# Kernel tuning notes

Hardware: AMD Instinct MI355X
Metric: run time of the kernel (lower is better)

The kernel has to match this reference:

```python
import jax, jax.numpy as jnp
from jax import lax
import numpy as np

DIM, DT_RANK, D_INNER, D_STATE = 256, 16, 256, 16

def _ssm_params(key, d, dt_rank, d_inner, n):
    k1, k2, k3 = jax.random.split(key, 3)
    Wdbc = jax.random.normal(k1, (d, dt_rank + 2 * n), jnp.float32) * 0.02
    Wdt = jax.random.normal(k2, (dt_rank, d_inner), jnp.float32) * 0.02
    bdt = jax.random.normal(k3, (d_inner,), jnp.float32) * 0.02
    Alog = jnp.log(jnp.tile(jnp.arange(1, n + 1, dtype=jnp.float32), (d_inner, 1)))
    D = jnp.ones((d_inner,), jnp.float32)
    return Wdbc, Wdt, bdt, Alog, D

def setup_inputs() -> dict:
    key = jax.random.key(0)
    ks = jax.random.split(key, 10)
    x = jax.random.normal(ks[0], (4, 4096, DIM), jnp.float32)
    ln_g = jnp.ones((DIM,), jnp.float32)
    ln_b = jnp.zeros((DIM,), jnp.float32)
    Wp = jax.random.normal(ks[1], (DIM, DIM), jnp.float32) * 0.02
    bp = jnp.zeros((DIM,), jnp.float32)
    Wcf = jax.random.normal(ks[2], (DIM, DIM), jnp.float32) * 0.02  # conv1d k=1 == pointwise matmul
    bcf = jnp.zeros((DIM,), jnp.float32)
    Wcb = jax.random.normal(ks[3], (DIM, DIM), jnp.float32) * 0.02
    bcb = jnp.zeros((DIM,), jnp.float32)
    Wdbc_f, Wdt_f, bdt_f, Alog_f, D_f = _ssm_params(ks[4], DIM, DT_RANK, D_INNER, D_STATE)
    Wdbc_b, Wdt_b, bdt_b, Alog_b, D_b = _ssm_params(ks[5], DIM, DT_RANK, D_INNER, D_STATE)
    return dict(x=x, ln_g=ln_g, ln_b=ln_b, Wp=Wp, bp=bp, Wcf=Wcf, bcf=bcf, Wcb=Wcb, bcb=bcb,
                Wdbc_f=Wdbc_f, Wdt_f=Wdt_f, bdt_f=bdt_f, Alog_f=Alog_f, D_f=D_f,
                Wdbc_b=Wdbc_b, Wdt_b=Wdt_b, bdt_b=bdt_b, Alog_b=Alog_b, D_b=D_b)

def _layernorm(x, g, b, eps=1e-5):
    mu = jnp.mean(x, -1, keepdims=True)
    var = jnp.var(x, -1, keepdims=True)
    return (x - mu) * lax.rsqrt(var + eps) * g + b

def _selective_scan(x, delta, A, B, C, D):
    # x, delta: [b,s,d]; A: [d,n]; B, C: [b,s,n]; D: [d]
    deltaA = jnp.exp(delta[..., None] * A)              # [b,s,d,n]
    BX = delta[..., None] * B[:, :, None, :] * x[..., None]  # [b,s,d,n]
    dA = jnp.moveaxis(deltaA, 1, 0)
    bx = jnp.moveaxis(BX, 1, 0)
    def step(h, inp):
        dA_t, bx_t = inp
        h = dA_t * h + bx_t
        return h, h
    h0 = jnp.zeros_like(dA[0])
    _, hs = lax.scan(step, h0, (dA, bx))                # [s,b,d,n]
    hs = jnp.moveaxis(hs, 0, 1)                          # [b,s,d,n]
    y = jnp.einsum('bsdn,bsn->bsd', hs, C) + D * x
    return y

def _ssm(x, Wdbc, Wdt, bdt, Alog, D):
    A = -jnp.exp(Alog)
    dbc = x @ Wdbc
    dt_r, B, C = jnp.split(dbc, [DT_RANK, DT_RANK + D_STATE], axis=-1)
    delta = jax.nn.softplus(dt_r @ Wdt + bdt)
    return _selective_scan(x, delta, A, B, C, D)

def _process(x, Wc, bc, Wdbc, Wdt, bdt, Alog, D):
    x = jax.nn.softplus(x @ Wc.T + bc)  # Conv1d k=1: out[e] = sum_d W[e,d] x[d] + b[e]
    return _ssm(x, Wdbc, Wdt, bdt, Alog, D)

def reference(x, ln_g, ln_b, Wp, bp, Wcf, bcf, Wcb, bcb,
              Wdbc_f, Wdt_f, bdt_f, Alog_f, D_f,
              Wdbc_b, Wdt_b, bdt_b, Alog_b, D_b):
    skip = x
    xn = _layernorm(x, ln_g, ln_b)
    z1 = xn @ Wp + bp  # proj used for both z1 and x (same layer twice)
    xp = z1
    x1 = jax.nn.silu(_process(xp, Wcf, bcf, Wdbc_f, Wdt_f, bdt_f, Alog_f, D_f))
    x2r = _process(jnp.flip(xp, 1), Wcb, bcb, Wdbc_b, Wdt_b, bdt_b, Alog_b, D_b)
    x2 = jax.nn.silu(jnp.flip(x2r, 1))
    z = jax.nn.silu(z1)
    return x1 * z + x2 * z + skip
```

## Files before the change

### kernel.cpp

```cpp
#include <hip/hip_runtime.h>
#include <math.h>

#define SB 4
#define SS 4096
#define SD 256
#define SN 16
#define ROWS 16
#define NRB 1024
#define NCH 128
#define CHL 32

#define BM 128
#define BN 64
#define BK 64
#define LDT 72

#define MBM 64
#define MLDZ 264
#define MLDT 72
#define MLDE 68

typedef __attribute__((ext_vector_type(8))) short bf16x8;
typedef __attribute__((ext_vector_type(4))) float f32x4;

__device__ __forceinline__ unsigned short f2bf(float f){
    unsigned int u = __float_as_uint(f);
    u += 0x7FFFu + ((u >> 16) & 1u);
    return (unsigned short)(u >> 16);
}
__device__ __forceinline__ float bf2f(unsigned short u){
    return __uint_as_float(((unsigned int)u) << 16);
}
__device__ __forceinline__ float softplus_f(float x){
    return fmaxf(x, 0.f) + __logf(1.f + __expf(-fabsf(x)));
}
__device__ __forceinline__ float silu_f(float x){
    return x * __builtin_amdgcn_rcpf(1.f + __expf(-x));
}

__global__ __launch_bounds__(256)
void k_prep(const float* __restrict__ Wp,
            const float* __restrict__ Wcf, const float* __restrict__ Wcb,
            const float* __restrict__ Wdbc0, const float* __restrict__ Wdt0,
            const float* __restrict__ Wdbc1, const float* __restrict__ Wdt1,
            unsigned short* __restrict__ WpT, unsigned short* __restrict__ Wc,
            unsigned short* __restrict__ G3W)
{
    int idx = blockIdx.x*256 + threadIdx.x;
    if (idx < 65536){
        int n = idx >> 8, k = idx & 255;
        WpT[idx] = f2bf(Wp[k*256 + n]);
    } else if (idx < 65536 + 131072){
        int j = idx - 65536;
        Wc[j] = f2bf(j < 65536 ? Wcf[j] : Wcb[j - 65536]);
    } else {
        int j = idx - 196608;
        int dir = j / 81920; int r = j - dir*81920;
        int n = r >> 8, d = r & 255;
        const float* Wdbc = dir ? Wdbc1 : Wdbc0;
        const float* Wdt  = dir ? Wdt1  : Wdt0;
        float v;
        if (n < 256){
            v = 0.f;
            #pragma unroll
            for (int q = 0; q < 16; ++q)
                v = fmaf(Wdbc[d*48 + q], Wdt[q*256 + n], v);
        } else if (n < 272) v = Wdbc[d*48 + 16 + (n-256)];
        else if (n < 288)   v = Wdbc[d*48 + 32 + (n-272)];
        else                v = 0.f;
        G3W[(size_t)dir*81920 + r] = f2bf(v);
    }
}

__global__ __launch_bounds__(256)
void k_ln(const float* __restrict__ x, const float* __restrict__ g,
          const float* __restrict__ bln, unsigned short* __restrict__ xnbf){
    int row0 = blockIdx.x * ROWS;
    int tid = threadIdx.x; int w = tid >> 6; int lane = tid & 63;
    #pragma unroll
    for (int rep = 0; rep < 4; ++rep){
        int j = rep*4 + w;
        const float* xr = x + (size_t)(row0 + j)*SD;
        float4 v = *(const float4*)(xr + lane*4);
        float s = v.x + v.y + v.z + v.w;
        #pragma unroll
        for (int off = 32; off; off >>= 1) s += __shfl_xor(s, off, 64);
        float mu = s * (1.f/256.f);
        float d0 = v.x-mu, d1 = v.y-mu, d2 = v.z-mu, d3 = v.w-mu;
        float q = d0*d0 + d1*d1 + d2*d2 + d3*d3;
        #pragma unroll
        for (int off = 32; off; off >>= 1) q += __shfl_xor(q, off, 64);
        float rstd = rsqrtf(q*(1.f/256.f) + 1e-5f);
        float4 gg = *(const float4*)(g + lane*4);
        float4 bb = *(const float4*)(bln + lane*4);
        ushort4 o;
        o.x = f2bf(d0*rstd*gg.x + bb.x);
        o.y = f2bf(d1*rstd*gg.y + bb.y);
        o.z = f2bf(d2*rstd*gg.z + bb.z);
        o.w = f2bf(d3*rstd*gg.w + bb.w);
        *(ushort4*)(xnbf + (size_t)(row0+j)*SD + lane*4) = o;
    }
}

__global__ __launch_bounds__(256, 5)
void k_gemm0(const unsigned short* __restrict__ A,
             const unsigned short* __restrict__ Bt,
             const float* __restrict__ bias0,
             unsigned short* __restrict__ obf)
{
    __shared__ unsigned short sMem[(BM + BN) * LDT];
    unsigned short (*sA)[LDT] = (unsigned short (*)[LDT])sMem;
    unsigned short (*sB)[LDT] = (unsigned short (*)[LDT])(sMem + BM*LDT);
    int ntile = blockIdx.x, mtile = blockIdx.y;
    int row0 = mtile * BM;
    int col0 = ntile * BN;

    int tid = threadIdx.x;
    uint4 ra[4], rb[2];
    auto gload = [&](int kt){
        int k0 = kt * BK;
        #pragma unroll
        for (int i = 0; i < 4; ++i){
            int idx = tid + i*256; int r = idx >> 3, kp = idx & 7;
            ra[i] = *(const uint4*)(A + (size_t)(row0 + r)*256 + k0 + kp*8);
        }
        #pragma unroll
        for (int i = 0; i < 2; ++i){
            int idx = tid + i*256; int r = idx >> 3, kp = idx & 7;
            rb[i] = *(const uint4*)(Bt + (size_t)(col0 + r)*256 + k0 + kp*8);
        }
    };
    auto swrite = [&](){
        #pragma unroll
        for (int i = 0; i < 4; ++i){
            int idx = tid + i*256; int r = idx >> 3, kp = idx & 7;
            *(uint4*)&sA[r][kp*8] = ra[i];
        }
        #pragma unroll
        for (int i = 0; i < 2; ++i){
            int idx = tid + i*256; int r = idx >> 3, kp = idx & 7;
            *(uint4*)&sB[r][kp*8] = rb[i];
        }
    };

    gload(0); swrite(); __syncthreads();

    int lane = tid & 63, w = tid >> 6;
    int wr = w >> 1, wc = w & 1;
    int lr = lane & 15, hi = lane >> 4;

    f32x4 acc[4][2];
    #pragma unroll
    for (int mf = 0; mf < 4; ++mf)
        #pragma unroll
        for (int nf = 0; nf < 2; ++nf)
            acc[mf][nf] = f32x4{0.f, 0.f, 0.f, 0.f};

    for (int kt = 0; kt < 4; ++kt){
        if (kt < 3) gload(kt + 1);
        #pragma unroll
        for (int kk = 0; kk < BK; kk += 32){
            bf16x8 af[4], bfr[2];
            #pragma unroll
            for (int mf = 0; mf < 4; ++mf)
                af[mf] = *(const bf16x8*)&sA[wr*64 + mf*16 + lr][kk + hi*8];
            #pragma unroll
            for (int nf = 0; nf < 2; ++nf)
                bfr[nf] = *(const bf16x8*)&sB[wc*32 + nf*16 + lr][kk + hi*8];
            #pragma unroll
            for (int mf = 0; mf < 4; ++mf)
                #pragma unroll
                for (int nf = 0; nf < 2; ++nf)
                    acc[mf][nf] = __builtin_amdgcn_mfma_f32_16x16x32_bf16(
                        af[mf], bfr[nf], acc[mf][nf], 0, 0, 0);
        }
        if (kt < 3){
            __syncthreads();
            swrite();
            __syncthreads();
        }
    }

    __syncthreads();
    unsigned short (*sOut)[LDT] = (unsigned short (*)[LDT])sMem;
    #pragma unroll
    for (int mf = 0; mf < 4; ++mf){
        #pragma unroll
        for (int nf = 0; nf < 2; ++nf){
            int col = col0 + wc*32 + nf*16 + lr;
            float bias = bias0[col];
            #pragma unroll
            for (int r = 0; r < 4; ++r)
                sOut[wr*64 + mf*16 + hi*4 + r][wc*32 + nf*16 + lr] =
                    f2bf(acc[mf][nf][r] + bias);
        }
    }
    __syncthreads();
    #pragma unroll
    for (int p = 0; p < 4; ++p){
        int chunk = tid + p*256;
        int r = chunk >> 3, cg = chunk & 7;
        uint4 v = *(const uint4*)&sOut[r][cg*8];
        *(uint4*)(obf + (size_t)(row0 + r)*256 + col0 + cg*8) = v;
    }
}

__global__ __launch_bounds__(256, 2)
void k_mid(const unsigned short* __restrict__ z1bf,
           const unsigned short* __restrict__ Wc,
           const unsigned short* __restrict__ G3W,
           const float* __restrict__ bc0, const float* __restrict__ bc1,
           const float* __restrict__ bdt0, const float* __restrict__ bdt1,
           unsigned short* __restrict__ xcbf,
           unsigned short* __restrict__ dg0, unsigned short* __restrict__ dg1,
           float* __restrict__ Bg0, float* __restrict__ Bg1,
           float* __restrict__ Cg0, float* __restrict__ Cg1)
{
    __shared__ unsigned short sZ[MBM*MLDZ];
    __shared__ unsigned short sX[MBM*MLDT];
    int mtile = blockIdx.x, dir = blockIdx.y;
    int row0 = mtile*MBM;
    int tid = threadIdx.x;
    int lane = tid & 63, w = tid >> 6;
    int wr = w >> 1, wc = w & 1;
    int lr = lane & 15, hi = lane >> 4;

    {
        const uint4* src = (const uint4*)(z1bf + (size_t)row0*256);
        #pragma unroll
        for (int p = 0; p < 8; ++p){
            int idx = tid + p*256;
            int r = idx >> 5, cq = idx & 31;
            *(uint4*)&sZ[r*MLDZ + cq*8] = src[idx];
        }
    }
    __syncthreads();

    const float* bcp  = dir ? bc1  : bc0;
    const float* bdtp = dir ? bdt1 : bdt0;
    unsigned short* dgp = dir ? dg1 : dg0;
    const unsigned short* Wcp = Wc + (size_t)dir*65536;
    const unsigned short* Gp  = G3W + (size_t)dir*81920;

    f32x4 acc2[5][2][2];
    #pragma unroll
    for (int t5 = 0; t5 < 5; ++t5)
        #pragma unroll
        for (int mf = 0; mf < 2; ++mf)
            #pragma unroll
            for (int nf = 0; nf < 2; ++nf)
                acc2[t5][mf][nf] = f32x4{0.f,0.f,0.f,0.f};

    #pragma unroll 1
    for (int nt1 = 0; nt1 < 4; ++nt1){
        f32x4 acc1[2][2];
        #pragma unroll
        for (int mf = 0; mf < 2; ++mf)
            #pragma unroll
            for (int nf = 0; nf < 2; ++nf)
                acc1[mf][nf] = f32x4{0.f,0.f,0.f,0.f};
        #pragma unroll
        for (int kt = 0; kt < 4; ++kt){
            #pragma unroll
            for (int kk = 0; kk < 64; kk += 32){
                bf16x8 wf0 = *(const bf16x8*)(Wcp + (size_t)(nt1*64 + wc*32 +      lr)*256 + kt*64 + kk + hi*8);
                bf16x8 wf1 = *(const bf16x8*)(Wcp + (size_t)(nt1*64 + wc*32 + 16 + lr)*256 + kt*64 + kk + hi*8);
                bf16x8 zf0 = *(const bf16x8*)&sZ[(wr*32 +      lr)*MLDZ + kt*64 + kk + hi*8];
                bf16x8 zf1 = *(const bf16x8*)&sZ[(wr*32 + 16 + lr)*MLDZ + kt*64 + kk + hi*8];
                acc1[0][0] = __builtin_amdgcn_mfma_f32_16x16x32_bf16(wf0, zf0, acc1[0][0], 0,0,0);
                acc1[0][1] = __builtin_amdgcn_mfma_f32_16x16x32_bf16(wf1, zf0, acc1[0][1], 0,0,0);
                acc1[1][0] = __builtin_amdgcn_mfma_f32_16x16x32_bf16(wf0, zf1, acc1[1][0], 0,0,0);
                acc1[1][1] = __builtin_amdgcn_mfma_f32_16x16x32_bf16(wf1, zf1, acc1[1][1], 0,0,0);
            }
        }
        __syncthreads();
        #pragma unroll
        for (int mf = 0; mf < 2; ++mf){
            #pragma unroll
            for (int nf = 0; nf < 2; ++nf){
                float4 bb = *(const float4*)(bcp + nt1*64 + wc*32 + nf*16 + hi*4);
                ushort4 o;
                o.x = f2bf(softplus_f(acc1[mf][nf][0] + bb.x));
                o.y = f2bf(softplus_f(acc1[mf][nf][1] + bb.y));
                o.z = f2bf(softplus_f(acc1[mf][nf][2] + bb.z));
                o.w = f2bf(softplus_f(acc1[mf][nf][3] + bb.w));
                *(ushort4*)&sX[(wr*32 + mf*16 + lr)*MLDT + wc*32 + nf*16 + hi*4] = o;
            }
        }
        __syncthreads();
        #pragma unroll
        for (int p = 0; p < 2; ++p){
            int idx = tid + p*256; int r = idx>>3, c8 = idx&7;
            *(uint4*)(xcbf + (size_t)(row0 + r)*512 + dir*256 + nt1*64 + c8*8) =
                *(const uint4*)&sX[r*MLDT + c8*8];
        }
        bf16x8 af[2][2];
        #pragma unroll
        for (int mf = 0; mf < 2; ++mf)
            #pragma unroll
            for (int k2 = 0; k2 < 2; ++k2)
                af[mf][k2] = *(const bf16x8*)&sX[(wr*32 + mf*16 + lr)*MLDT + k2*32 + hi*8];
        #pragma unroll
        for (int nt2 = 0; nt2 < 5; ++nt2){
            #pragma unroll
            for (int k2 = 0; k2 < 2; ++k2){
                bf16x8 gf0 = *(const bf16x8*)(Gp + (size_t)(nt2*64 + wc*32 +      lr)*256 + nt1*64 + k2*32 + hi*8);
                bf16x8 gf1 = *(const bf16x8*)(Gp + (size_t)(nt2*64 + wc*32 + 16 + lr)*256 + nt1*64 + k2*32 + hi*8);
                acc2[nt2][0][0] = __builtin_amdgcn_mfma_f32_16x16x32_bf16(af[0][k2], gf0, acc2[nt2][0][0], 0,0,0);
                acc2[nt2][0][1] = __builtin_amdgcn_mfma_f32_16x16x32_bf16(af[0][k2], gf1, acc2[nt2][0][1], 0,0,0);
                acc2[nt2][1][0] = __builtin_amdgcn_mfma_f32_16x16x32_bf16(af[1][k2], gf0, acc2[nt2][1][0], 0,0,0);
                acc2[nt2][1][1] = __builtin_amdgcn_mfma_f32_16x16x32_bf16(af[1][k2], gf1, acc2[nt2][1][1], 0,0,0);
            }
        }
    }

    float* sE = (float*)sZ;
    #pragma unroll
    for (int nt2 = 0; nt2 < 5; ++nt2){
        __syncthreads();
        #pragma unroll
        for (int mf = 0; mf < 2; ++mf)
            #pragma unroll
            for (int nf = 0; nf < 2; ++nf)
                #pragma unroll
                for (int r = 0; r < 4; ++r)
                    sE[(wr*32 + mf*16 + hi*4 + r)*MLDE + wc*32 + nf*16 + lr] =
                        acc2[nt2][mf][nf][r];
        __syncthreads();
        if (nt2 < 4){
            #pragma unroll
            for (int p = 0; p < 2; ++p){
                int idx = tid + p*256; int r = idx>>3, c8 = idx&7;
                float4 v0 = *(const float4*)&sE[r*MLDE + c8*8];
                float4 v1 = *(const float4*)&sE[r*MLDE + c8*8 + 4];
                int col = nt2*64 + c8*8;
                float4 b0 = *(const float4*)(bdtp + col);
                float4 b1 = *(const float4*)(bdtp + col + 4);
                ushort4 o0, o1;
                o0.x = f2bf(softplus_f(v0.x + b0.x));
                o0.y = f2bf(softplus_f(v0.y + b0.y));
                o0.z = f2bf(softplus_f(v0.z + b0.z));
                o0.w = f2bf(softplus_f(v0.w + b0.w));
                o1.x = f2bf(softplus_f(v1.x + b1.x));
                o1.y = f2bf(softplus_f(v1.y + b1.y));
                o1.z = f2bf(softplus_f(v1.z + b1.z));
                o1.w = f2bf(softplus_f(v1.w + b1.w));
                ushort4 pk[2] = {o0, o1};
                *(uint4*)(dgp + (size_t)(row0 + r)*SD + col) = *(const uint4*)pk;
            }
        } else {
            float* Bp = dir ? Bg1 : Bg0;
            float* Cp = dir ? Cg1 : Cg0;
            int r = tid >> 2, q = tid & 3;
            float4 bv = *(const float4*)&sE[r*MLDE + q*4];
            float4 cv = *(const float4*)&sE[r*MLDE + 16 + q*4];
            *(float4*)(Bp + (size_t)(row0 + r)*SN + q*4) = bv;
            *(float4*)(Cp + (size_t)(row0 + r)*SN + q*4) = cv;
        }
    }
}

__global__ __launch_bounds__(256)
void k_scan_p1(const unsigned short* __restrict__ xcbf,
               const unsigned short* __restrict__ dg0, const float* __restrict__ B0, const float* __restrict__ Al0,
               const unsigned short* __restrict__ dg1, const float* __restrict__ B1, const float* __restrict__ Al1,
               float* __restrict__ hend, float* __restrict__ sdl)
{
    __shared__ float sB[CHL*SN];
    int blk = blockIdx.x;
    int c = blk & (NCH-1); int dir = (blk>>7) & 1; int b = blk>>8;
    const unsigned short* dg = dir ? dg1 : dg0;
    const float* Bg   = dir ? B1  : B0;
    const float* Alog = dir ? Al1 : Al0;
    const unsigned short* xc = xcbf + dir*256;
    int d = threadIdx.x;
    #pragma unroll
    for (int k = 0; k < 2; ++k){
        int li = threadIdx.x + k*256;
        int i = li >> 4, n = li & 15;
        int tau = c*CHL + i;
        int t = dir ? (SS-1-tau) : tau;
        sB[li] = Bg[((size_t)b*SS + t)*SN + n];
    }
    float A[SN];
    #pragma unroll
    for (int k = 0; k < 4; ++k){
        float4 al = *(const float4*)(Alog + d*SN + k*4);
        A[k*4+0] = -__expf(al.x); A[k*4+1] = -__expf(al.y);
        A[k*4+2] = -__expf(al.z); A[k*4+3] = -__expf(al.w);
    }
    __syncthreads();
    int t0 = dir ? (SS-1 - c*CHL) : (c*CHL);
    const unsigned short* pd = dg + ((size_t)b*SS + t0)*SD + d;
    const unsigned short* px = xc + ((size_t)b*SS + t0)*512 + d;
    int strided = dir ? -SD : SD;
    int stridex = dir ? -512 : 512;
    float h[SN];
    #pragma unroll
    for (int n = 0; n < SN; ++n) h[n] = 0.f;
    float sumdl = 0.f;
    float dl = bf2f(*pd), xv = bf2f(*px);
    for (int i = 0; i < CHL; ++i){
        float dlN = 0.f, xvN = 0.f;
        if (i+1 < CHL){ pd += strided; px += stridex; dlN = bf2f(*pd); xvN = bf2f(*px); }
        sumdl += dl;
        float dlx = dl * xv;
        const float4* b4 = (const float4*)&sB[i*SN];
        #pragma unroll
        for (int k = 0; k < 4; ++k){
            float4 bb = b4[k];
            h[k*4+0] = fmaf(__expf(dl*A[k*4+0]), h[k*4+0], bb.x*dlx);
            h[k*4+1] = fmaf(__expf(dl*A[k*4+1]), h[k*4+1], bb.y*dlx);
            h[k*4+2] = fmaf(__expf(dl*A[k*4+2]), h[k*4+2], bb.z*dlx);
            h[k*4+3] = fmaf(__expf(dl*A[k*4+3]), h[k*4+3], bb.w*dlx);
        }
        dl = dlN; xv = xvN;
    }
    size_t base = (((size_t)(b*2+dir)*NCH + c)*SD + d)*SN;
    #pragma unroll
    for (int k = 0; k < 4; ++k)
        *(float4*)(hend + base + k*4) = make_float4(h[k*4+0],h[k*4+1],h[k*4+2],h[k*4+3]);
    sdl[((size_t)(b*2+dir)*NCH + c)*SD + d] = sumdl;
}

__global__ __launch_bounds__(256)
void k_chain(const float* __restrict__ Al0, const float* __restrict__ Al1,
             float* hend, const float* __restrict__ sdl)
{
    int gidx = blockIdx.x*256 + threadIdx.x;
    int n = gidx & 15; int d = (gidx >> 4) & 255; int dirb = gidx >> 12;
    const float* Alog = (dirb & 1) ? Al1 : Al0;
    float A = -__expf(Alog[d*SN + n]);
    float H = 0.f;
    const size_t cs = (size_t)SD*SN;
    size_t idx  = (size_t)dirb*NCH*cs + (size_t)d*SN + n;
    size_t sidx = (size_t)dirb*NCH*SD + d;
    float he[4], sd[4];
    #pragma unroll
    for (int k = 0; k < 4; ++k){
        he[k] = hend[idx + (size_t)k*cs];
        sd[k] = sdl[sidx + (size_t)k*SD];
    }
    for (int cg = 0; cg < NCH; cg += 4){
        float heN[4] = {0.f,0.f,0.f,0.f};
        float sdN[4] = {0.f,0.f,0.f,0.f};
        if (cg + 4 < NCH){
            #pragma unroll
            for (int k = 0; k < 4; ++k){
                heN[k] = hend[idx + (size_t)(k+4)*cs];
                sdN[k] = sdl[sidx + (size_t)(k+4)*SD];
            }
        }
        #pragma unroll
        for (int k = 0; k < 4; ++k){
            hend[idx + (size_t)k*cs] = H;
            H = fmaf(__expf(A*sd[k]), H, he[k]);
        }
        #pragma unroll
        for (int k = 0; k < 4; ++k){ he[k] = heN[k]; sd[k] = sdN[k]; }
        idx += 4*cs; sidx += 4*SD;
    }
}

__global__ __launch_bounds__(256)
void k_scan_p2f(const unsigned short* __restrict__ xcbf,
                const unsigned short* __restrict__ dg0, const float* __restrict__ B0,
                const float* __restrict__ C0, const float* __restrict__ Al0,
                const float* __restrict__ Dv0,
                const unsigned short* __restrict__ dg1, const float* __restrict__ B1,
                const float* __restrict__ C1, const float* __restrict__ Al1,
                const float* __restrict__ Dv1,
                const float* __restrict__ hin,
                const unsigned short* __restrict__ z1bf,
                const float* __restrict__ x,
                float* __restrict__ out)
{
    __shared__ float yL[CHL*SD];
    __shared__ float sB0[CHL*SN], sC0[CHL*SN], sB1[CHL*SN], sC1[CHL*SN];
    int blk = blockIdx.x;
    int c = blk & (NCH-1); int b = blk >> 7;
    int d = threadIdx.x;
    #pragma unroll
    for (int k = 0; k < 2; ++k){
        int li = threadIdx.x + k*256;
        int i = li >> 4, n = li & 15;
        int tF = c*CHL + i;
        int tR = c*CHL + (CHL-1) - i;
        sB0[li] = B0[((size_t)b*SS + tF)*SN + n];
        sC0[li] = C0[((size_t)b*SS + tF)*SN + n];
        sB1[li] = B1[((size_t)b*SS + tR)*SN + n];
        sC1[li] = C1[((size_t)b*SS + tR)*SN + n];
    }
    __syncthreads();

    {
        float A[SN];
        #pragma unroll
        for (int k = 0; k < 4; ++k){
            float4 al = *(const float4*)(Al0 + d*SN + k*4);
            A[k*4+0] = -__expf(al.x); A[k*4+1] = -__expf(al.y);
            A[k*4+2] = -__expf(al.z); A[k*4+3] = -__expf(al.w);
        }
        float h[SN];
        size_t base = (((size_t)(b*2+0)*NCH + c)*SD + d)*SN;
        #pragma unroll
        for (int k = 0; k < 4; ++k){
            float4 hv = *(const float4*)(hin + base + k*4);
            h[k*4+0]=hv.x; h[k*4+1]=hv.y; h[k*4+2]=hv.z; h[k*4+3]=hv.w;
        }
        float Dd = Dv0[d];
        for (int i = 0; i < CHL; ++i){
            size_t rowb = (size_t)b*SS + c*CHL + i;
            float dl = bf2f(dg0[rowb*SD + d]);
            float xv = bf2f(xcbf[rowb*512 + d]);
            float dlx = dl * xv;
            float yv = Dd * xv;
            const float4* b4 = (const float4*)&sB0[i*SN];
            const float4* c4 = (const float4*)&sC0[i*SN];
            #pragma unroll
            for (int k = 0; k < 4; ++k){
                float4 bb = b4[k];
                float4 cc = c4[k];
                h[k*4+0] = fmaf(__expf(dl*A[k*4+0]), h[k*4+0], bb.x*dlx);
                yv = fmaf(h[k*4+0], cc.x, yv);
                h[k*4+1] = fmaf(__expf(dl*A[k*4+1]), h[k*4+1], bb.y*dlx);
                yv = fmaf(h[k*4+1], cc.y, yv);
                h[k*4+2] = fmaf(__expf(dl*A[k*4+2]), h[k*4+2], bb.z*dlx);
                yv = fmaf(h[k*4+2], cc.z, yv);
                h[k*4+3] = fmaf(__expf(dl*A[k*4+3]), h[k*4+3], bb.w*dlx);
                yv = fmaf(h[k*4+3], cc.w, yv);
            }
            yL[i*SD + d] = yv;
        }
    }
    {
        float A[SN];
        #pragma unroll
        for (int k = 0; k < 4; ++k){
            float4 al = *(const float4*)(Al1 + d*SN + k*4);
            A[k*4+0] = -__expf(al.x); A[k*4+1] = -__expf(al.y);
            A[k*4+2] = -__expf(al.z); A[k*4+3] = -__expf(al.w);
        }
        float h[SN];
        size_t base = (((size_t)(b*2+1)*NCH + (NCH-1-c))*SD + d)*SN;
        #pragma unroll
        for (int k = 0; k < 4; ++k){
            float4 hv = *(const float4*)(hin + base + k*4);
            h[k*4+0]=hv.x; h[k*4+1]=hv.y; h[k*4+2]=hv.z; h[k*4+3]=hv.w;
        }
        float Dd = Dv1[d];
        for (int ip = 0; ip < CHL; ++ip){
            int iloc = (CHL-1) - ip;
            size_t rowb = (size_t)b*SS + c*CHL + iloc;
            float dl = bf2f(dg1[rowb*SD + d]);
            float xv = bf2f(xcbf[rowb*512 + 256 + d]);
            float dlx = dl * xv;
            float yv = Dd * xv;
            const float4* b4 = (const float4*)&sB1[ip*SN];
            const float4* c4 = (const float4*)&sC1[ip*SN];
            #pragma unroll
            for (int k = 0; k < 4; ++k){
                float4 bb = b4[k];
                float4 cc = c4[k];
                h[k*4+0] = fmaf(__expf(dl*A[k*4+0]), h[k*4+0], bb.x*dlx);
                yv = fmaf(h[k*4+0], cc.x, yv);
                h[k*4+1] = fmaf(__expf(dl*A[k*4+1]), h[k*4+1], bb.y*dlx);
                yv = fmaf(h[k*4+1], cc.y, yv);
                h[k*4+2] = fmaf(__expf(dl*A[k*4+2]), h[k*4+2], bb.z*dlx);
                yv = fmaf(h[k*4+2], cc.z, yv);
                h[k*4+3] = fmaf(__expf(dl*A[k*4+3]), h[k*4+3], bb.w*dlx);
                yv = fmaf(h[k*4+3], cc.w, yv);
            }
            float y0v = yL[iloc*SD + d];
            float zv = bf2f(z1bf[rowb*SD + d]);
            float xo = x[rowb*SD + d];
            out[rowb*SD + d] = (silu_f(y0v) + silu_f(yv)) * silu_f(zv) + xo;
        }
    }
}

extern "C" void kernel_launch(void* const* d_in, const int* in_sizes, int n_in,
                              void* d_out, int out_size, void* d_ws, size_t ws_size,
                              hipStream_t stream) {
    const float* x     = (const float*)d_in[0];
    const float* ln_g  = (const float*)d_in[1];
    const float* ln_b  = (const float*)d_in[2];
    const float* Wp    = (const float*)d_in[3];
    const float* bp    = (const float*)d_in[4];
    const float* Wcf   = (const float*)d_in[5];
    const float* bcf   = (const float*)d_in[6];
    const float* Wcb   = (const float*)d_in[7];
    const float* bcb   = (const float*)d_in[8];
    const float* Wdbc_f= (const float*)d_in[9];
    const float* Wdt_f = (const float*)d_in[10];
    const float* bdt_f = (const float*)d_in[11];
    const float* Alog_f= (const float*)d_in[12];
    const float* D_f   = (const float*)d_in[13];
    const float* Wdbc_b= (const float*)d_in[14];
    const float* Wdt_b = (const float*)d_in[15];
    const float* bdt_b = (const float*)d_in[16];
    const float* Alog_b= (const float*)d_in[17];
    const float* D_b   = (const float*)d_in[18];
    float* out = (float*)d_out;

    float* ws = (float*)d_ws;
    const size_t NTOK  = (size_t)SB*SS;
    const size_t SZ_BD = NTOK*SD;
    const size_t SZ_BN = NTOK*SN;
    size_t off = 0;
    float* dgr   = ws + off; off += SZ_BD;
    unsigned short* dg0 = (unsigned short*)dgr;
    unsigned short* dg1 = dg0 + SZ_BD;
    float* Bg0   = ws + off; off += SZ_BN;
    float* Bg1   = ws + off; off += SZ_BN;
    float* Cg0   = ws + off; off += SZ_BN;
    float* Cg1   = ws + off; off += SZ_BN;
    float* regA  = ws + off; off += SZ_BD;
    unsigned short* xnbf = (unsigned short*)regA;
    unsigned short* z1bf = xnbf + SZ_BD;
    float* regB  = ws + off; off += SZ_BD;
    unsigned short* xcbf = (unsigned short*)regB;
    float* hend  = ws + off; off += SZ_BD;
    float* sdl   = ws + off; off += (size_t)8*NCH*SD;
    unsigned short* WpT  = (unsigned short*)(ws + off); off += 65536/2;
    unsigned short* Wc   = (unsigned short*)(ws + off); off += 131072/2;
    unsigned short* G3W  = (unsigned short*)(ws + off); off += 163840/2;

    k_prep<<<1408, 256, 0, stream>>>(Wp, Wcf, Wcb, Wdbc_f, Wdt_f, Wdbc_b, Wdt_b,
                                     WpT, Wc, G3W);
    k_ln<<<NRB, 256, 0, stream>>>(x, ln_g, ln_b, xnbf);
    k_gemm0<<<dim3(4,128), 256, 0, stream>>>(xnbf, WpT, bp, z1bf);
    k_mid<<<dim3(256,2), 256, 0, stream>>>(z1bf, Wc, G3W,
        bcf, bcb, bdt_f, bdt_b, xcbf,
        dg0, dg1, Bg0, Bg1, Cg0, Cg1);
    k_scan_p1<<<1024, 256, 0, stream>>>(xcbf, dg0, Bg0, Alog_f,
                                        dg1, Bg1, Alog_b, hend, sdl);
    k_chain<<<128, 256, 0, stream>>>(Alog_f, Alog_b, hend, sdl);
    k_scan_p2f<<<512, 256, 0, stream>>>(xcbf,
        dg0, Bg0, Cg0, Alog_f, D_f,
        dg1, Bg1, Cg1, Alog_b, D_b,
        hend, z1bf, x, out);
}
```

Measured before the change: 165.0 us.

## Restructure k_mid into 32-row tiles with transposed MFMA and direct epilogue stores

Halves the k_mid row tile to 32 and doubles the grid. Each wave now owns a 16-column slice of both chained GEMMs, so the first GEMM runs in one pass over all four column tiles before a single barrier. Swapping the MFMA operand order puts the accumulators in token-major layout, so dt/B/C are written straight from registers instead of staged through an LDS float buffer with repeated barriers. This trades fewer barriers and more blocks per CU for more per-block weight reads from global memory and smaller, possibly less coalesced output stores.

```diff
diff --git a/kernel.cpp b/kernel.cpp
--- a/kernel.cpp
+++ b/kernel.cpp
@@ -15,10 +15,8 @@
 #define BK 64
 #define LDT 72
 
-#define MBM 64
+#define MBM 32
 #define MLDZ 264
-#define MLDT 72
-#define MLDE 68
 
 typedef __attribute__((ext_vector_type(8))) short bf16x8;
 typedef __attribute__((ext_vector_type(4))) float f32x4;
@@ -205,7 +203,7 @@
     }
 }
 
-__global__ __launch_bounds__(256, 2)
+__global__ __launch_bounds__(256, 4)
 void k_mid(const unsigned short* __restrict__ z1bf,
            const unsigned short* __restrict__ Wc,
            const unsigned short* __restrict__ G3W,
@@ -217,18 +215,17 @@
            float* __restrict__ Cg0, float* __restrict__ Cg1)
 {
     __shared__ unsigned short sZ[MBM*MLDZ];
-    __shared__ unsigned short sX[MBM*MLDT];
+    __shared__ unsigned short sX[MBM*MLDZ];
     int mtile = blockIdx.x, dir = blockIdx.y;
     int row0 = mtile*MBM;
     int tid = threadIdx.x;
     int lane = tid & 63, w = tid >> 6;
-    int wr = w >> 1, wc = w & 1;
     int lr = lane & 15, hi = lane >> 4;
 
     {
         const uint4* src = (const uint4*)(z1bf + (size_t)row0*256);
         #pragma unroll
-        for (int p = 0; p < 8; ++p){
+        for (int p = 0; p < 4; ++p){
             int idx = tid + p*256;
             int r = idx >> 5, cq = idx & 31;
             *(uint4*)&sZ[r*MLDZ + cq*8] = src[idx];
@@ -242,120 +239,105 @@
     const unsigned short* Wcp = Wc + (size_t)dir*65536;
     const unsigned short* Gp  = G3W + (size_t)dir*81920;
 
-    f32x4 acc2[5][2][2];
+    f32x4 acc1[4][2];
+    #pragma unroll
+    for (int nt1 = 0; nt1 < 4; ++nt1)
+        #pragma unroll
+        for (int mf = 0; mf < 2; ++mf)
+            acc1[nt1][mf] = f32x4{0.f,0.f,0.f,0.f};
+    #pragma unroll
+    for (int kt = 0; kt < 4; ++kt){
+        #pragma unroll
+        for (int kk2 = 0; kk2 < 2; ++kk2){
+            int ko = kt*64 + kk2*32 + hi*8;
+            bf16x8 wf[4];
+            #pragma unroll
+            for (int nt1 = 0; nt1 < 4; ++nt1)
+                wf[nt1] = *(const bf16x8*)(Wcp + (size_t)(nt1*64 + w*16 + lr)*256 + ko);
+            bf16x8 zf0 = *(const bf16x8*)&sZ[(     lr)*MLDZ + ko];
+            bf16x8 zf1 = *(const bf16x8*)&sZ[(16 + lr)*MLDZ + ko];
+            #pragma unroll
+            for (int nt1 = 0; nt1 < 4; ++nt1){
+                acc1[nt1][0] = __builtin_amdgcn_mfma_f32_16x16x32_bf16(wf[nt1], zf0, acc1[nt1][0], 0,0,0);
+                acc1[nt1][1] = __builtin_amdgcn_mfma_f32_16x16x32_bf16(wf[nt1], zf1, acc1[nt1][1], 0,0,0);
+            }
+        }
+    }
+    #pragma unroll
+    for (int nt1 = 0; nt1 < 4; ++nt1){
+        #pragma unroll
+        for (int mf = 0; mf < 2; ++mf){
+            float4 bb = *(const float4*)(bcp + nt1*64 + w*16 + hi*4);
+            ushort4 o;
+            o.x = f2bf(softplus_f(acc1[nt1][mf][0] + bb.x));
+            o.y = f2bf(softplus_f(acc1[nt1][mf][1] + bb.y));
+            o.z = f2bf(softplus_f(acc1[nt1][mf][2] + bb.z));
+            o.w = f2bf(softplus_f(acc1[nt1][mf][3] + bb.w));
+            *(ushort4*)&sX[(mf*16 + lr)*MLDZ + nt1*64 + w*16 + hi*4] = o;
+        }
+    }
+    __syncthreads();
+    {
+        #pragma unroll
+        for (int p = 0; p < 4; ++p){
+            int idx = tid + p*256;
+            int r = idx >> 5, cq = idx & 31;
+            *(uint4*)(xcbf + (size_t)(row0 + r)*512 + dir*256 + cq*8) =
+                *(const uint4*)&sX[r*MLDZ + cq*8];
+        }
+    }
+
+    f32x4 acc2[5][2];
     #pragma unroll
     for (int t5 = 0; t5 < 5; ++t5)
         #pragma unroll
         for (int mf = 0; mf < 2; ++mf)
-            #pragma unroll
-            for (int nf = 0; nf < 2; ++nf)
-                acc2[t5][mf][nf] = f32x4{0.f,0.f,0.f,0.f};
-
-    #pragma unroll 1
+            acc2[t5][mf] = f32x4{0.f,0.f,0.f,0.f};
+    #pragma unroll
     for (int nt1 = 0; nt1 < 4; ++nt1){
-        f32x4 acc1[2][2];
+        bf16x8 af[2][2];
         #pragma unroll
         for (int mf = 0; mf < 2; ++mf)
             #pragma unroll
-            for (int nf = 0; nf < 2; ++nf)
-                acc1[mf][nf] = f32x4{0.f,0.f,0.f,0.f};
-        #pragma unroll
-        for (int kt = 0; kt < 4; ++kt){
-            #pragma unroll
-            for (int kk = 0; kk < 64; kk += 32){
-                bf16x8 wf0 = *(const bf16x8*)(Wcp + (size_t)(nt1*64 + wc*32 +      lr)*256 + kt*64 + kk + hi*8);
-                bf16x8 wf1 = *(const bf16x8*)(Wcp + (size_t)(nt1*64 + wc*32 + 16 + lr)*256 + kt*64 + kk + hi*8);
-                bf16x8 zf0 = *(const bf16x8*)&sZ[(wr*32 +      lr)*MLDZ + kt*64 + kk + hi*8];
-                bf16x8 zf1 = *(const bf16x8*)&sZ[(wr*32 + 16 + lr)*MLDZ + kt*64 + kk + hi*8];
-                acc1[0][0] = __builtin_amdgcn_mfma_f32_16x16x32_bf16(wf0, zf0, acc1[0][0], 0,0,0);
-                acc1[0][1] = __builtin_amdgcn_mfma_f32_16x16x32_bf16(wf1, zf0, acc1[0][1], 0,0,0);
-                acc1[1][0] = __builtin_amdgcn_mfma_f32_16x16x32_bf16(wf0, zf1, acc1[1][0], 0,0,0);
-                acc1[1][1] = __builtin_amdgcn_mfma_f32_16x16x32_bf16(wf1, zf1, acc1[1][1], 0,0,0);
+            for (int k2 = 0; k2 < 2; ++k2)
+                af[mf][k2] = *(const bf16x8*)&sX[(mf*16 + lr)*MLDZ + nt1*64 + k2*32 + hi*8];
+        #pragma unroll
+        for (int k2 = 0; k2 < 2; ++k2){
+            int ko = nt1*64 + k2*32 + hi*8;
+            bf16x8 gf[5];
+            #pragma unroll
+            for (int nt2 = 0; nt2 < 5; ++nt2)
+                gf[nt2] = *(const bf16x8*)(Gp + (size_t)(nt2*64 + w*16 + lr)*256 + ko);
+            #pragma unroll
+            for (int nt2 = 0; nt2 < 5; ++nt2){
+                acc2[nt2][0] = __builtin_amdgcn_mfma_f32_16x16x32_bf16(gf[nt2], af[0][k2], acc2[nt2][0], 0,0,0);
+                acc2[nt2][1] = __builtin_amdgcn_mfma_f32_16x16x32_bf16(gf[nt2], af[1][k2], acc2[nt2][1], 0,0,0);
             }
         }
-        __syncthreads();
+    }
+
+    #pragma unroll
+    for (int nt2 = 0; nt2 < 4; ++nt2){
         #pragma unroll
         for (int mf = 0; mf < 2; ++mf){
-            #pragma unroll
-            for (int nf = 0; nf < 2; ++nf){
-                float4 bb = *(const float4*)(bcp + nt1*64 + wc*32 + nf*16 + hi*4);
-                ushort4 o;
-                o.x = f2bf(softplus_f(acc1[mf][nf][0] + bb.x));
-                o.y = f2bf(softplus_f(acc1[mf][nf][1] + bb.y));
-                o.z = f2bf(softplus_f(acc1[mf][nf][2] + bb.z));
-                o.w = f2bf(softplus_f(acc1[mf][nf][3] + bb.w));
-                *(ushort4*)&sX[(wr*32 + mf*16 + lr)*MLDT + wc*32 + nf*16 + hi*4] = o;
-            }
-        }
-        __syncthreads();
-        #pragma unroll
-        for (int p = 0; p < 2; ++p){
-            int idx = tid + p*256; int r = idx>>3, c8 = idx&7;
-            *(uint4*)(xcbf + (size_t)(row0 + r)*512 + dir*256 + nt1*64 + c8*8) =
-                *(const uint4*)&sX[r*MLDT + c8*8];
-        }
-        bf16x8 af[2][2];
-        #pragma unroll
-        for (int mf = 0; mf < 2; ++mf)
-            #pragma unroll
-            for (int k2 = 0; k2 < 2; ++k2)
-                af[mf][k2] = *(const bf16x8*)&sX[(wr*32 + mf*16 + lr)*MLDT + k2*32 + hi*8];
-        #pragma unroll
-        for (int nt2 = 0; nt2 < 5; ++nt2){
-            #pragma unroll
-            for (int k2 = 0; k2 < 2; ++k2){
-                bf16x8 gf0 = *(const bf16x8*)(Gp + (size_t)(nt2*64 + wc*32 +      lr)*256 + nt1*64 + k2*32 + hi*8);
-                bf16x8 gf1 = *(const bf16x8*)(Gp + (size_t)(nt2*64 + wc*32 + 16 + lr)*256 + nt1*64 + k2*32 + hi*8);
-                acc2[nt2][0][0] = __builtin_amdgcn_mfma_f32_16x16x32_bf16(af[0][k2], gf0, acc2[nt2][0][0], 0,0,0);
-                acc2[nt2][0][1] = __builtin_amdgcn_mfma_f32_16x16x32_bf16(af[0][k2], gf1, acc2[nt2][0][1], 0,0,0);
-                acc2[nt2][1][0] = __builtin_amdgcn_mfma_f32_16x16x32_bf16(af[1][k2], gf0, acc2[nt2][1][0], 0,0,0);
-                acc2[nt2][1][1] = __builtin_amdgcn_mfma_f32_16x16x32_bf16(af[1][k2], gf1, acc2[nt2][1][1], 0,0,0);
-            }
-        }
-    }
-
-    float* sE = (float*)sZ;
-    #pragma unroll
-    for (int nt2 = 0; nt2 < 5; ++nt2){
-        __syncthreads();
-        #pragma unroll
-        for (int mf = 0; mf < 2; ++mf)
-            #pragma unroll
-            for (int nf = 0; nf < 2; ++nf)
-                #pragma unroll
-                for (int r = 0; r < 4; ++r)
-                    sE[(wr*32 + mf*16 + hi*4 + r)*MLDE + wc*32 + nf*16 + lr] =
-                        acc2[nt2][mf][nf][r];
-        __syncthreads();
-        if (nt2 < 4){
-            #pragma unroll
-            for (int p = 0; p < 2; ++p){
-                int idx = tid + p*256; int r = idx>>3, c8 = idx&7;
-                float4 v0 = *(const float4*)&sE[r*MLDE + c8*8];
-                float4 v1 = *(const float4*)&sE[r*MLDE + c8*8 + 4];
-                int col = nt2*64 + c8*8;
-                float4 b0 = *(const float4*)(bdtp + col);
-                float4 b1 = *(const float4*)(bdtp + col + 4);
-                ushort4 o0, o1;
-                o0.x = f2bf(softplus_f(v0.x + b0.x));
-                o0.y = f2bf(softplus_f(v0.y + b0.y));
-                o0.z = f2bf(softplus_f(v0.z + b0.z));
-                o0.w = f2bf(softplus_f(v0.w + b0.w));
-                o1.x = f2bf(softplus_f(v1.x + b1.x));
-                o1.y = f2bf(softplus_f(v1.y + b1.y));
-                o1.z = f2bf(softplus_f(v1.z + b1.z));
-                o1.w = f2bf(softplus_f(v1.w + b1.w));
-                ushort4 pk[2] = {o0, o1};
-                *(uint4*)(dgp + (size_t)(row0 + r)*SD + col) = *(const uint4*)pk;
-            }
-        } else {
-            float* Bp = dir ? Bg1 : Bg0;
-            float* Cp = dir ? Cg1 : Cg0;
-            int r = tid >> 2, q = tid & 3;
-            float4 bv = *(const float4*)&sE[r*MLDE + q*4];
-            float4 cv = *(const float4*)&sE[r*MLDE + 16 + q*4];
-            *(float4*)(Bp + (size_t)(row0 + r)*SN + q*4) = bv;
-            *(float4*)(Cp + (size_t)(row0 + r)*SN + q*4) = cv;
+            int tok = row0 + mf*16 + lr;
+            int col = nt2*64 + w*16 + hi*4;
+            float4 bb = *(const float4*)(bdtp + col);
+            ushort4 o;
+            o.x = f2bf(softplus_f(acc2[nt2][mf][0] + bb.x));
+            o.y = f2bf(softplus_f(acc2[nt2][mf][1] + bb.y));
+            o.z = f2bf(softplus_f(acc2[nt2][mf][2] + bb.z));
+            o.w = f2bf(softplus_f(acc2[nt2][mf][3] + bb.w));
+            *(ushort4*)(dgp + (size_t)tok*SD + col) = o;
+        }
+    }
+    if (w < 2){
+        float* P = (w == 0) ? (dir ? Bg1 : Bg0) : (dir ? Cg1 : Cg0);
+        #pragma unroll
+        for (int mf = 0; mf < 2; ++mf){
+            int tok = row0 + mf*16 + lr;
+            float4 v = { acc2[4][mf][0], acc2[4][mf][1], acc2[4][mf][2], acc2[4][mf][3] };
+            *(float4*)(P + (size_t)tok*SN + hi*4) = v;
         }
     }
 }
@@ -630,7 +612,7 @@
                                      WpT, Wc, G3W);
     k_ln<<<NRB, 256, 0, stream>>>(x, ln_g, ln_b, xnbf);
     k_gemm0<<<dim3(4,128), 256, 0, stream>>>(xnbf, WpT, bp, z1bf);
-    k_mid<<<dim3(256,2), 256, 0, stream>>>(z1bf, Wc, G3W,
+    k_mid<<<dim3(512,2), 256, 0, stream>>>(z1bf, Wc, G3W,
         bcf, bcb, bdt_f, bdt_b, xcbf,
         dg0, dg1, Bg0, Bg1, Cg0, Cg1);
     k_scan_p1<<<1024, 256, 0, stream>>>(xcbf, dg0, Bg0, Alog_f,
```

After: 158.3 us. 4.0% less time.
